# Kernel optimization log

Hardware: AMD Instinct MI355X
Metric: run time of the kernel (lower is better)

Reference implementation:

```python
import jax, jax.numpy as jnp
import numpy as np

RADIUS = 0.25  # module init arg


def _spp(x):
    """Spatial pyramid max pooling over the (K=8, C) plane.
    x: [B, N, 8, C] -> [B, N, 21] (4x4 + 2x2 + 1x1 bins)."""
    B, N, K, C = x.shape
    outs = []
    for h, w in ((4, 4), (2, 2), (1, 1)):
        r = x.reshape(B, N, h, K // h, w, C // w)
        outs.append(r.max(axis=(3, 5)).reshape(B, N, h * w))
    return jnp.concatenate(outs, axis=-1)


def _pointsift_select(xyz, radius):
    """Octant-wise nearest-neighbor selection. xyz: [Bp, N, 3] -> idx [Bp, N, 8]."""
    Bp, N, _ = xyz.shape
    judge = radius * radius
    # diff[b, n, m] = xyz[b, m] - xyz[b, n]  (point m relative to centroid n)
    diff = xyz[:, None, :, :] - xyz[:, :, None, :]          # [Bp, N, N, 3]
    dist = jnp.sum(diff * diff, axis=-1)                     # [Bp, N, N]
    octw = jnp.array([4, 2, 1], dtype=jnp.int32)
    sub = jnp.sum((diff + 1.0).astype(jnp.int32) * octw, -1)  # [Bp, N, N] octant id
    valid = (dist > 1e-10) & (dist < judge)
    eye = jnp.eye(N, dtype=bool)                             # self entry gets judge_dist
    idxs = []
    for i in range(8):
        d_i = jnp.where(valid & (sub == i), dist, 1e10)
        d_i = jnp.where(eye, judge, d_i)
        idxs.append(jnp.argmin(d_i, axis=-1))                # first-min, matches torch
    return jnp.stack(idxs, axis=-1)                          # [Bp, N, 8]


def setup_inputs() -> dict:
    key = jax.random.key(0)
    ks = jax.random.split(key, 7)
    C = 256
    x = jax.random.uniform(ks[0], (2, 2, 2048, 3), dtype=jnp.float32)
    w1 = jax.random.normal(ks[1], (C, 3), dtype=jnp.float32) * 0.05
    b1 = jax.random.normal(ks[2], (C,), dtype=jnp.float32) * 0.05
    w2 = jax.random.normal(ks[3], (C, C), dtype=jnp.float32) * 0.05
    b2 = jax.random.normal(ks[4], (C,), dtype=jnp.float32) * 0.05
    w3 = jax.random.normal(ks[5], (C, C), dtype=jnp.float32) * 0.05
    b3 = jax.random.normal(ks[6], (C,), dtype=jnp.float32) * 0.05
    return {"x": x, "w1": w1, "b1": b1, "w2": w2, "b2": b2, "w3": w3, "b3": b3}


def reference(x, w1, b1, w2, b2, w3, b3):
    B, T, N, _ = x.shape
    xyz = x.reshape(B * T, N, 3)
    idx = _pointsift_select(xyz, RADIUS)                     # [Bp, N, 8]
    b_idx = jnp.arange(B * T)[:, None, None]
    grouped = xyz[b_idx, idx] - xyz[:, :, None, :]           # [Bp, N, 8, 3] relative coords
    # three stacked 1x1 convs (no nonlinearity, per original Sequential)
    h = jnp.einsum('bnkc,oc->bnko', grouped, w1) + b1
    h = jnp.einsum('bnkc,oc->bnko', h, w2) + b2
    h = jnp.einsum('bnkc,oc->bnko', h, w3) + b3              # [Bp, N, 8, C]
    out = _spp(h)                                            # [Bp, N, 21]
    return out.reshape(B, T, N, -1)
```

## Files before the change

### kernel.cpp

```cpp
#include <hip/hip_runtime.h>

#define NPTS 2048
#define CCH  256
#define CAP  320
#define CAPU (CAP - 64)

template <int CTRL>
__device__ __forceinline__ float dppf(float v) {
    return __int_as_float(__builtin_amdgcn_update_dpp(
        0, __float_as_int(v), CTRL, 0xF, 0xF, true));
}
__device__ __forceinline__ float row16_max(float v) {
    v = fmaxf(v, dppf<0xB1>(v));
    v = fmaxf(v, dppf<0x4E>(v));
    v = fmaxf(v, dppf<0x141>(v));
    v = fmaxf(v, dppf<0x140>(v));
    return v;
}
__device__ __forceinline__ float row16_min(float v) {
    v = fminf(v, dppf<0xB1>(v));
    v = fminf(v, dppf<0x4E>(v));
    v = fminf(v, dppf<0x141>(v));
    v = fminf(v, dppf<0x140>(v));
    return v;
}
__device__ __forceinline__ float row16_sum(float v) {
    v += dppf<0xB1>(v);
    v += dppf<0x4E>(v);
    v += dppf<0x141>(v);
    v += dppf<0x140>(v);
    return v;
}
__device__ __forceinline__ float wave_sum(float v) {
    v = row16_sum(v);
    v += __shfl_xor(v, 16, 64);
    v += __shfl_xor(v, 32, 64);
    return v;
}


__global__ __launch_bounds__(256) void prep_kernel(
    const float* __restrict__ w1, const float* __restrict__ b1,
    const float* __restrict__ w2, const float* __restrict__ b2,
    const float* __restrict__ w3, const float* __restrict__ b3,
    float* __restrict__ ws)
{
    __shared__ float  w3row[CCH];
    __shared__ float4 wpart[4];
    int o = blockIdx.x, c = threadIdx.x;

    float w3c = w3[o * CCH + c];
    w3row[c] = w3c;
    __syncthreads();

    float a0 = 0.f, a1 = 0.f, a2 = 0.f, a3 = 0.f;
    const float* w2c = w2 + c;
    for (int k = 0; k < CCH; k += 4) {
        a0 = fmaf(w3row[k + 0], w2c[(k + 0) * CCH], a0);
        a1 = fmaf(w3row[k + 1], w2c[(k + 1) * CCH], a1);
        a2 = fmaf(w3row[k + 2], w2c[(k + 2) * CCH], a2);
        a3 = fmaf(w3row[k + 3], w2c[(k + 3) * CCH], a3);
    }
    float acc = (a0 + a1) + (a2 + a3);

    float4 v = make_float4(acc * w1[c * 3 + 0],
                           acc * w1[c * 3 + 1],
                           acc * w1[c * 3 + 2],
                           fmaf(acc, b1[c], w3c * b2[c]));
    v.x = wave_sum(v.x);
    v.y = wave_sum(v.y);
    v.z = wave_sum(v.z);
    v.w = wave_sum(v.w);
    if ((c & 63) == 0) wpart[c >> 6] = v;
    __syncthreads();
    if (c == 0) {
        float4 p0 = wpart[0], p1 = wpart[1], p2 = wpart[2], p3 = wpart[3];
        ws[o * 3 + 0] = (p0.x + p1.x) + (p2.x + p3.x);
        ws[o * 3 + 1] = (p0.y + p1.y) + (p2.y + p3.y);
        ws[o * 3 + 2] = (p0.z + p1.z) + (p2.z + p3.z);
        ws[3 * CCH + o] = (p0.w + p1.w) + (p2.w + p3.w) + b3[o];
    }
}

__global__ __launch_bounds__(1024) void pointsift_kernel(
    const float* __restrict__ x,
    const float* __restrict__ ws,
    float* __restrict__ out)
{
    __shared__ float4 sx4[NPTS];
    __shared__ unsigned short slist[16][CAP];

    int batch = blockIdx.x >> 7;
    int n0    = (blockIdx.x & 127) * 16;
    const float* xb = x + (size_t)batch * NPTS * 3;

    for (int i = threadIdx.x; i < NPTS; i += 1024) {
        float3 p = *(const float3*)(xb + 3 * i);
        sx4[i] = make_float4(p.x, p.y, p.z, 0.f);
    }

    int wave = threadIdx.x >> 6;
    int lane = threadIdx.x & 63;
    int n = n0 + wave;

    float3 cpt = *(const float3*)(xb + 3 * n);
    float cx = cpt.x, cy = cpt.y, cz = cpt.z;

    __syncthreads();

    unsigned short* slw = slist[wave];

    unsigned cnt = 0;
#pragma unroll 4
    for (int m = lane; m < NPTS; m += 64) {
        float4 p = sx4[m];
        float dx = p.x - cx, dy = p.y - cy, dz = p.z - cz;
        float d2 = __fadd_rn(__fadd_rn(__fmul_rn(dx, dx), __fmul_rn(dy, dy)),
                             __fmul_rn(dz, dz));
        bool valid = (d2 > 1e-10f) && (d2 < 0.0625f);
        unsigned long long mask = __ballot(valid);
        if (valid && cnt <= CAPU) {
            unsigned below = __builtin_amdgcn_mbcnt_hi(
                (unsigned)(mask >> 32),
                __builtin_amdgcn_mbcnt_lo((unsigned)mask, 0u));
            slw[cnt + below] = (unsigned short)m;
        }
        cnt += (unsigned)__popcll(mask);
    }

    float bd[8];
    int   bi[8];
#pragma unroll
    for (int i = 0; i < 8; ++i) { bd[i] = __builtin_inff(); bi[i] = n; }

    if (cnt <= CAPU) {
        int cn = (int)cnt;
        for (int t = lane; t < cn; t += 64) {
            int m = slw[t];
            float4 p = sx4[m];
            float dx = p.x - cx, dy = p.y - cy, dz = p.z - cz;
            float d2 = __fadd_rn(__fadd_rn(__fmul_rn(dx, dx), __fmul_rn(dy, dy)),
                                 __fmul_rn(dz, dz));
            int oct = 4 * (int)(dx + 1.0f) + 2 * (int)(dy + 1.0f) + (int)(dz + 1.0f);
#pragma unroll
            for (int i = 0; i < 8; ++i) {
                bool upd = (oct == i) && (d2 < bd[i]);
                bd[i] = upd ? d2 : bd[i];
                bi[i] = upd ? m : bi[i];
            }
        }
    } else {
        for (int m = lane; m < NPTS; m += 64) {
            float4 p = sx4[m];
            float dx = p.x - cx, dy = p.y - cy, dz = p.z - cz;
            float d2 = __fadd_rn(__fadd_rn(__fmul_rn(dx, dx), __fmul_rn(dy, dy)),
                                 __fmul_rn(dz, dz));
            bool valid = (d2 > 1e-10f) && (d2 < 0.0625f);
            int oct = 4 * (int)(dx + 1.0f) + 2 * (int)(dy + 1.0f) + (int)(dz + 1.0f);
#pragma unroll
            for (int i = 0; i < 8; ++i) {
                bool upd = valid && (oct == i) && (d2 < bd[i]);
                bd[i] = upd ? d2 : bd[i];
                bi[i] = upd ? m : bi[i];
            }
        }
    }

    int nidx[8];
#pragma unroll
    for (int i = 0; i < 8; ++i) {
        float mv = row16_min(bd[i]);
        mv = fminf(mv, __shfl_xor(mv, 16, 64));
        mv = fminf(mv, __shfl_xor(mv, 32, 64));
        unsigned long long mk = __ballot(bd[i] == mv);
        if (__popcll(mk) == 1) {
            nidx[i] = __builtin_amdgcn_readlane(bi[i], (int)__builtin_ctzll(mk));
        } else {
            int mm = (bd[i] == mv) ? bi[i] : 0x7FFFFFFF;
#pragma unroll
            for (int s = 32; s > 0; s >>= 1) {
                int o = __shfl_xor(mm, s, 64);
                mm = o < mm ? o : mm;
            }
            nidx[i] = mm;
        }
    }

    const float4* wsv = (const float4*)ws;
    float4 wa = wsv[lane * 3 + 0];
    float4 wb = wsv[lane * 3 + 1];
    float4 wc = wsv[lane * 3 + 2];
    float4 be = ((const float4*)(ws + 3 * CCH))[lane];
    float w[4][3] = {{wa.x, wa.y, wa.z}, {wa.w, wb.x, wb.y},
                     {wb.z, wb.w, wc.x}, {wc.y, wc.z, wc.w}};
    float bev[4] = {be.x, be.y, be.z, be.w};

    float m16[4];
#pragma unroll
    for (int i = 0; i < 4; ++i) m16[i] = -__builtin_inff();
#pragma unroll
    for (int k = 0; k < 8; ++k) {
        float4 p = sx4[nidx[k]];
        float gx = p.x - cx, gy = p.y - cy, gz = p.z - cz;
#pragma unroll
        for (int q = 0; q < 4; ++q) {
            float h = fmaf(gx, w[q][0], fmaf(gy, w[q][1], fmaf(gz, w[q][2], bev[q])));
            m16[k >> 1] = fmaxf(m16[k >> 1], h);
        }
    }

    float t[4], u[4];
#pragma unroll
    for (int i = 0; i < 4; ++i) {
        m16[i] = row16_max(m16[i]);
        t[i] = fmaxf(m16[i], __shfl_xor(m16[i], 16, 64));
        u[i] = fmaxf(t[i], __shfl_xor(t[i], 32, 64));
    }

    float* op = out + ((size_t)batch * NPTS + n) * 21;
    if ((lane & 15) == 0) {
        int j = lane >> 4;
#pragma unroll
        for (int i = 0; i < 4; ++i)
            op[i * 4 + j] = m16[i];
    }
    if (lane == 0 || lane == 32) {
        int j2 = lane >> 5;
        op[16 + 0 * 2 + j2] = fmaxf(t[0], t[1]);
        op[16 + 1 * 2 + j2] = fmaxf(t[2], t[3]);
    }
    if (lane == 0) {
        op[20] = fmaxf(fmaxf(u[0], u[1]), fmaxf(u[2], u[3]));
    }
}

extern "C" void kernel_launch(void* const* d_in, const int* in_sizes, int n_in,
                              void* d_out, int out_size, void* d_ws, size_t ws_size,
                              hipStream_t stream) {
    const float* x  = (const float*)d_in[0];
    const float* w1 = (const float*)d_in[1];
    const float* b1 = (const float*)d_in[2];
    const float* w2 = (const float*)d_in[3];
    const float* b2 = (const float*)d_in[4];
    const float* w3 = (const float*)d_in[5];
    const float* b3 = (const float*)d_in[6];
    float* out = (float*)d_out;
    float* ws  = (float*)d_ws;

    prep_kernel<<<CCH, CCH, 0, stream>>>(w1, b1, w2, b2, w3, b3, ws);

    int Bp = in_sizes[0] / (NPTS * 3);
    pointsift_kernel<<<Bp * (NPTS / 16), 1024, 0, stream>>>(x, ws, out);
}
```

Measured before the change: 26.83 us.

## Bin points into 4x4x4 uniform grid and scan only neighboring cells

Adds a binning pass to the prep kernel that counting-sorts each batch's points into a 4x4x4 grid of cells of size 0.25, storing sorted coordinates, original ids and cell start offsets in the workspace. The main kernel then scans only the 3x3x3 neighbouring cells of each centroid instead of all 2048 points when building the candidate list. Ties are broken on the original index so results still match first-min argmin order. The cost is an extra sort pass folded into the existing prep launch, plus reading neighbour coordinates from global memory in the final stage.

```diff
diff --git a/kernel.cpp b/kernel.cpp
--- a/kernel.cpp
+++ b/kernel.cpp
@@ -4,6 +4,10 @@
 #define CCH  256
 #define CAP  320
 #define CAPU (CAP - 64)
+
+#define STARTS_OFF 4096
+#define IDS_OFF    6144
+#define CRD_OFF    22528
 
 template <int CTRL>
 __device__ __forceinline__ float dppf(float v) {
@@ -38,47 +42,107 @@
     return v;
 }
 
-
-__global__ __launch_bounds__(256) void prep_kernel(
+__device__ __forceinline__ int cell_coord(float v) {
+    int c = (int)(v * 4.0f);
+    return min(3, max(0, c));
+}
+
+__global__ __launch_bounds__(256) void prep_bin_kernel(
+    const float* __restrict__ x,
     const float* __restrict__ w1, const float* __restrict__ b1,
     const float* __restrict__ w2, const float* __restrict__ b2,
     const float* __restrict__ w3, const float* __restrict__ b3,
-    float* __restrict__ ws)
+    float* __restrict__ ws, int Bp)
 {
     __shared__ float  w3row[CCH];
     __shared__ float4 wpart[4];
-    int o = blockIdx.x, c = threadIdx.x;
-
-    float w3c = w3[o * CCH + c];
-    w3row[c] = w3c;
+    __shared__ unsigned hist[64];
+    __shared__ unsigned curs[64];
+    __shared__ unsigned short cellOf[NPTS];
+
+    int tid = threadIdx.x;
+
+    if ((int)blockIdx.x < CCH) {
+        int o = blockIdx.x, c = tid;
+        float w3c = w3[o * CCH + c];
+        w3row[c] = w3c;
+        __syncthreads();
+
+        float a0 = 0.f, a1 = 0.f, a2 = 0.f, a3 = 0.f;
+        const float* w2c = w2 + c;
+        for (int k = 0; k < CCH; k += 4) {
+            a0 = fmaf(w3row[k + 0], w2c[(k + 0) * CCH], a0);
+            a1 = fmaf(w3row[k + 1], w2c[(k + 1) * CCH], a1);
+            a2 = fmaf(w3row[k + 2], w2c[(k + 2) * CCH], a2);
+            a3 = fmaf(w3row[k + 3], w2c[(k + 3) * CCH], a3);
+        }
+        float acc = (a0 + a1) + (a2 + a3);
+
+        float4 v = make_float4(acc * w1[c * 3 + 0],
+                               acc * w1[c * 3 + 1],
+                               acc * w1[c * 3 + 2],
+                               fmaf(acc, b1[c], w3c * b2[c]));
+        v.x = wave_sum(v.x);
+        v.y = wave_sum(v.y);
+        v.z = wave_sum(v.z);
+        v.w = wave_sum(v.w);
+        if ((c & 63) == 0) wpart[c >> 6] = v;
+        __syncthreads();
+        if (c == 0) {
+            float4 p0 = wpart[0], p1 = wpart[1], p2 = wpart[2], p3 = wpart[3];
+            ws[o * 3 + 0] = (p0.x + p1.x) + (p2.x + p3.x);
+            ws[o * 3 + 1] = (p0.y + p1.y) + (p2.y + p3.y);
+            ws[o * 3 + 2] = (p0.z + p1.z) + (p2.z + p3.z);
+            ws[3 * CCH + o] = (p0.w + p1.w) + (p2.w + p3.w) + b3[o];
+        }
+        return;
+    }
+
+    int b = blockIdx.x - CCH;
+    if (b >= Bp) return;
+    const float* xb = x + (size_t)b * NPTS * 3;
+
+    if (tid < 64) hist[tid] = 0;
     __syncthreads();
 
-    float a0 = 0.f, a1 = 0.f, a2 = 0.f, a3 = 0.f;
-    const float* w2c = w2 + c;
-    for (int k = 0; k < CCH; k += 4) {
-        a0 = fmaf(w3row[k + 0], w2c[(k + 0) * CCH], a0);
-        a1 = fmaf(w3row[k + 1], w2c[(k + 1) * CCH], a1);
-        a2 = fmaf(w3row[k + 2], w2c[(k + 2) * CCH], a2);
-        a3 = fmaf(w3row[k + 3], w2c[(k + 3) * CCH], a3);
-    }
-    float acc = (a0 + a1) + (a2 + a3);
-
-    float4 v = make_float4(acc * w1[c * 3 + 0],
-                           acc * w1[c * 3 + 1],
-                           acc * w1[c * 3 + 2],
-                           fmaf(acc, b1[c], w3c * b2[c]));
-    v.x = wave_sum(v.x);
-    v.y = wave_sum(v.y);
-    v.z = wave_sum(v.z);
-    v.w = wave_sum(v.w);
-    if ((c & 63) == 0) wpart[c >> 6] = v;
+    float3 pr[8];
+    int    cl[8];
+#pragma unroll 8
+    for (int j = 0; j < 8; ++j) {
+        int i = tid + 256 * j;
+        float3 p = *(const float3*)(xb + 3 * i);
+        pr[j] = p;
+        int c = (cell_coord(p.x) << 4) | (cell_coord(p.y) << 2) | cell_coord(p.z);
+        cl[j] = c;
+        cellOf[i] = (unsigned short)c;
+        atomicAdd(&hist[c], 1u);
+    }
     __syncthreads();
-    if (c == 0) {
-        float4 p0 = wpart[0], p1 = wpart[1], p2 = wpart[2], p3 = wpart[3];
-        ws[o * 3 + 0] = (p0.x + p1.x) + (p2.x + p3.x);
-        ws[o * 3 + 1] = (p0.y + p1.y) + (p2.y + p3.y);
-        ws[o * 3 + 2] = (p0.z + p1.z) + (p2.z + p3.z);
-        ws[3 * CCH + o] = (p0.w + p1.w) + (p2.w + p3.w) + b3[o];
+
+    if (tid < 64) {
+        unsigned v = hist[tid];
+        unsigned inc = v;
+#pragma unroll
+        for (int s = 1; s < 64; s <<= 1) {
+            unsigned o = __shfl_up(inc, s, 64);
+            if (tid >= s) inc += o;
+        }
+        unsigned excl = inc - v;
+        curs[tid] = excl;
+        unsigned* st = (unsigned*)((char*)ws + STARTS_OFF) + b * 128;
+        st[tid] = excl;
+        if (tid == 63) st[64] = NPTS;
+    }
+    __syncthreads();
+
+    float4* crd         = (float4*)((char*)ws + CRD_OFF) + (size_t)b * NPTS;
+    unsigned short* ids = (unsigned short*)((char*)ws + IDS_OFF) + (size_t)b * NPTS;
+#pragma unroll 8
+    for (int j = 0; j < 8; ++j) {
+        int i = tid + 256 * j;
+        unsigned pos = atomicAdd(&curs[cl[j]], 1u);
+        crd[pos] = make_float4(pr[j].x, pr[j].y, pr[j].z, 0.f);
+        ids[pos] = (unsigned short)i;
     }
 }
 
@@ -87,17 +151,24 @@
     const float* __restrict__ ws,
     float* __restrict__ out)
 {
-    __shared__ float4 sx4[NPTS];
+    __shared__ float4 sc[NPTS];
+    __shared__ unsigned short sid[NPTS];
+    __shared__ unsigned sstart[65];
     __shared__ unsigned short slist[16][CAP];
 
     int batch = blockIdx.x >> 7;
     int n0    = (blockIdx.x & 127) * 16;
+
+    const float4* crd = (const float4*)((const char*)ws + CRD_OFF) + (size_t)batch * NPTS;
+    const unsigned short* idg = (const unsigned short*)((const char*)ws + IDS_OFF) + (size_t)batch * NPTS;
+    const unsigned* stg = (const unsigned*)((const char*)ws + STARTS_OFF) + batch * 128;
     const float* xb = x + (size_t)batch * NPTS * 3;
 
     for (int i = threadIdx.x; i < NPTS; i += 1024) {
-        float3 p = *(const float3*)(xb + 3 * i);
-        sx4[i] = make_float4(p.x, p.y, p.z, 0.f);
-    }
+        sc[i]  = crd[i];
+        sid[i] = idg[i];
+    }
+    if (threadIdx.x < 65) sstart[threadIdx.x] = stg[threadIdx.x];
 
     int wave = threadIdx.x >> 6;
     int lane = threadIdx.x & 63;
@@ -108,24 +179,40 @@
 
     __syncthreads();
 
+    int ccx = cell_coord(cx), ccy = cell_coord(cy), ccz = cell_coord(cz);
+    int zlo = ccz > 0 ? ccz - 1 : 0;
+    int zhi = ccz < 3 ? ccz + 1 : 3;
+
     unsigned short* slw = slist[wave];
 
     unsigned cnt = 0;
-#pragma unroll 4
-    for (int m = lane; m < NPTS; m += 64) {
-        float4 p = sx4[m];
-        float dx = p.x - cx, dy = p.y - cy, dz = p.z - cz;
-        float d2 = __fadd_rn(__fadd_rn(__fmul_rn(dx, dx), __fmul_rn(dy, dy)),
-                             __fmul_rn(dz, dz));
-        bool valid = (d2 > 1e-10f) && (d2 < 0.0625f);
-        unsigned long long mask = __ballot(valid);
-        if (valid && cnt <= CAPU) {
-            unsigned below = __builtin_amdgcn_mbcnt_hi(
-                (unsigned)(mask >> 32),
-                __builtin_amdgcn_mbcnt_lo((unsigned)mask, 0u));
-            slw[cnt + below] = (unsigned short)m;
-        }
-        cnt += (unsigned)__popcll(mask);
+    for (int di = -1; di <= 1; ++di) {
+        int a = ccx + di;
+        if ((unsigned)a > 3u) continue;
+        for (int dj = -1; dj <= 1; ++dj) {
+            int bcol = ccy + dj;
+            if ((unsigned)bcol > 3u) continue;
+            int base = (a << 4) | (bcol << 2);
+            unsigned s0 = sstart[base + zlo];
+            unsigned e0 = sstart[base + zhi + 1];
+            for (unsigned p0 = s0; p0 < e0; p0 += 64) {
+                unsigned pos = p0 + lane;
+                bool inb = pos < e0;
+                float4 p = sc[inb ? pos : 0];
+                float dx = p.x - cx, dy = p.y - cy, dz = p.z - cz;
+                float d2 = __fadd_rn(__fadd_rn(__fmul_rn(dx, dx), __fmul_rn(dy, dy)),
+                                     __fmul_rn(dz, dz));
+                bool valid = inb && (d2 > 1e-10f) && (d2 < 0.0625f);
+                unsigned long long mask = __ballot(valid);
+                if (valid && cnt <= CAPU) {
+                    unsigned below = __builtin_amdgcn_mbcnt_hi(
+                        (unsigned)(mask >> 32),
+                        __builtin_amdgcn_mbcnt_lo((unsigned)mask, 0u));
+                    slw[cnt + below] = (unsigned short)pos;
+                }
+                cnt += (unsigned)__popcll(mask);
+            }
+        }
     }
 
     float bd[8];
@@ -136,22 +223,25 @@
     if (cnt <= CAPU) {
         int cn = (int)cnt;
         for (int t = lane; t < cn; t += 64) {
-            int m = slw[t];
-            float4 p = sx4[m];
+            int pos = slw[t];
+            float4 p = sc[pos];
+            int m = sid[pos];
             float dx = p.x - cx, dy = p.y - cy, dz = p.z - cz;
             float d2 = __fadd_rn(__fadd_rn(__fmul_rn(dx, dx), __fmul_rn(dy, dy)),
                                  __fmul_rn(dz, dz));
             int oct = 4 * (int)(dx + 1.0f) + 2 * (int)(dy + 1.0f) + (int)(dz + 1.0f);
 #pragma unroll
             for (int i = 0; i < 8; ++i) {
-                bool upd = (oct == i) && (d2 < bd[i]);
+                bool upd = (oct == i) &&
+                           ((d2 < bd[i]) || ((d2 == bd[i]) && (m < bi[i])));
                 bd[i] = upd ? d2 : bd[i];
                 bi[i] = upd ? m : bi[i];
             }
         }
     } else {
-        for (int m = lane; m < NPTS; m += 64) {
-            float4 p = sx4[m];
+        for (int pos = lane; pos < NPTS; pos += 64) {
+            float4 p = sc[pos];
+            int m = sid[pos];
             float dx = p.x - cx, dy = p.y - cy, dz = p.z - cz;
             float d2 = __fadd_rn(__fadd_rn(__fmul_rn(dx, dx), __fmul_rn(dy, dy)),
                                  __fmul_rn(dz, dz));
@@ -159,7 +249,8 @@
             int oct = 4 * (int)(dx + 1.0f) + 2 * (int)(dy + 1.0f) + (int)(dz + 1.0f);
 #pragma unroll
             for (int i = 0; i < 8; ++i) {
-                bool upd = valid && (oct == i) && (d2 < bd[i]);
+                bool upd = valid && (oct == i) &&
+                           ((d2 < bd[i]) || ((d2 == bd[i]) && (m < bi[i])));
                 bd[i] = upd ? d2 : bd[i];
                 bi[i] = upd ? m : bi[i];
             }
@@ -200,7 +291,7 @@
     for (int i = 0; i < 4; ++i) m16[i] = -__builtin_inff();
 #pragma unroll
     for (int k = 0; k < 8; ++k) {
-        float4 p = sx4[nidx[k]];
+        float3 p = *(const float3*)(xb + 3 * nidx[k]);
         float gx = p.x - cx, gy = p.y - cy, gz = p.z - cz;
 #pragma unroll
         for (int q = 0; q < 4; ++q) {
@@ -247,8 +338,8 @@
     float* out = (float*)d_out;
     float* ws  = (float*)d_ws;
 
-    prep_kernel<<<CCH, CCH, 0, stream>>>(w1, b1, w2, b2, w3, b3, ws);
-
     int Bp = in_sizes[0] / (NPTS * 3);
+
+    prep_bin_kernel<<<CCH + Bp, CCH, 0, stream>>>(x, w1, b1, w2, b2, w3, b3, ws, Bp);
     pointsift_kernel<<<Bp * (NPTS / 16), 1024, 0, stream>>>(x, ws, out);
 }
```

After: 28.97 us. +8.0%, slower.

## Bin points into a 4x4x4 shared-memory grid to prune neighbor search

Applied to the files above, without the earlier changes.

Each block builds a 64-cell spatial histogram of the batch's points, prefix-sums it and scatters the points into cell-sorted order in shared memory. Each centroid wave then scans only the 3x3x3 neighboring cells instead of all 2048 points. Original indices are packed into the float4's w slot, and 64-bit (distance, index) keys keep first-min tie-breaking after the reorder. The prep kernel now computes two output channels per block, sharing the w2 loads. This adds atomics and extra barriers per block, and the gather at the end reads from global memory.

```diff
diff --git a/kernel.cpp b/kernel.cpp
--- a/kernel.cpp
+++ b/kernel.cpp
@@ -38,6 +38,11 @@
     return v;
 }
 
+__device__ __forceinline__ int cell_coord(float v) {
+    int c = (int)(v * 4.0f);
+    return min(3, max(0, c));
+}
+
 
 __global__ __launch_bounds__(256) void prep_kernel(
     const float* __restrict__ w1, const float* __restrict__ b1,
@@ -45,36 +50,55 @@
     const float* __restrict__ w3, const float* __restrict__ b3,
     float* __restrict__ ws)
 {
-    __shared__ float  w3row[CCH];
-    __shared__ float4 wpart[4];
-    int o = blockIdx.x, c = threadIdx.x;
-
-    float w3c = w3[o * CCH + c];
-    w3row[c] = w3c;
+    __shared__ float  w3row[2][CCH];
+    __shared__ float4 wpart[2][4];
+    int o0 = blockIdx.x * 2, c = threadIdx.x;
+
+    float w3c0 = w3[(o0 + 0) * CCH + c];
+    float w3c1 = w3[(o0 + 1) * CCH + c];
+    w3row[0][c] = w3c0;
+    w3row[1][c] = w3c1;
     __syncthreads();
 
     float a0 = 0.f, a1 = 0.f, a2 = 0.f, a3 = 0.f;
+    float b0 = 0.f, b1p = 0.f, b2p = 0.f, b3p = 0.f;
     const float* w2c = w2 + c;
     for (int k = 0; k < CCH; k += 4) {
-        a0 = fmaf(w3row[k + 0], w2c[(k + 0) * CCH], a0);
-        a1 = fmaf(w3row[k + 1], w2c[(k + 1) * CCH], a1);
-        a2 = fmaf(w3row[k + 2], w2c[(k + 2) * CCH], a2);
-        a3 = fmaf(w3row[k + 3], w2c[(k + 3) * CCH], a3);
-    }
-    float acc = (a0 + a1) + (a2 + a3);
-
-    float4 v = make_float4(acc * w1[c * 3 + 0],
-                           acc * w1[c * 3 + 1],
-                           acc * w1[c * 3 + 2],
-                           fmaf(acc, b1[c], w3c * b2[c]));
-    v.x = wave_sum(v.x);
-    v.y = wave_sum(v.y);
-    v.z = wave_sum(v.z);
-    v.w = wave_sum(v.w);
-    if ((c & 63) == 0) wpart[c >> 6] = v;
-    __syncthreads();
-    if (c == 0) {
-        float4 p0 = wpart[0], p1 = wpart[1], p2 = wpart[2], p3 = wpart[3];
+        float q0 = w2c[(k + 0) * CCH];
+        float q1 = w2c[(k + 1) * CCH];
+        float q2 = w2c[(k + 2) * CCH];
+        float q3 = w2c[(k + 3) * CCH];
+        a0 = fmaf(w3row[0][k + 0], q0, a0);
+        a1 = fmaf(w3row[0][k + 1], q1, a1);
+        a2 = fmaf(w3row[0][k + 2], q2, a2);
+        a3 = fmaf(w3row[0][k + 3], q3, a3);
+        b0  = fmaf(w3row[1][k + 0], q0, b0);
+        b1p = fmaf(w3row[1][k + 1], q1, b1p);
+        b2p = fmaf(w3row[1][k + 2], q2, b2p);
+        b3p = fmaf(w3row[1][k + 3], q3, b3p);
+    }
+    float accA = (a0 + a1) + (a2 + a3);
+    float accB = (b0 + b1p) + (b2p + b3p);
+
+    float w1x = w1[c * 3 + 0], w1y = w1[c * 3 + 1], w1z = w1[c * 3 + 2];
+    float b1c = b1[c], b2c = b2[c];
+
+    float4 vA = make_float4(accA * w1x, accA * w1y, accA * w1z,
+                            fmaf(accA, b1c, w3c0 * b2c));
+    float4 vB = make_float4(accB * w1x, accB * w1y, accB * w1z,
+                            fmaf(accB, b1c, w3c1 * b2c));
+    vA.x = wave_sum(vA.x); vA.y = wave_sum(vA.y);
+    vA.z = wave_sum(vA.z); vA.w = wave_sum(vA.w);
+    vB.x = wave_sum(vB.x); vB.y = wave_sum(vB.y);
+    vB.z = wave_sum(vB.z); vB.w = wave_sum(vB.w);
+    if ((c & 63) == 0) {
+        wpart[0][c >> 6] = vA;
+        wpart[1][c >> 6] = vB;
+    }
+    __syncthreads();
+    if (c < 2) {
+        int o = o0 + c;
+        float4 p0 = wpart[c][0], p1 = wpart[c][1], p2 = wpart[c][2], p3 = wpart[c][3];
         ws[o * 3 + 0] = (p0.x + p1.x) + (p2.x + p3.x);
         ws[o * 3 + 1] = (p0.y + p1.y) + (p2.y + p3.y);
         ws[o * 3 + 2] = (p0.z + p1.z) + (p2.z + p3.z);
@@ -87,20 +111,55 @@
     const float* __restrict__ ws,
     float* __restrict__ out)
 {
-    __shared__ float4 sx4[NPTS];
+    __shared__ float4 scrd[NPTS];
+    __shared__ unsigned sstart[66];
+    __shared__ unsigned shist[64];
+    __shared__ unsigned scur[64];
     __shared__ unsigned short slist[16][CAP];
 
+    int tid = threadIdx.x;
     int batch = blockIdx.x >> 7;
     int n0    = (blockIdx.x & 127) * 16;
     const float* xb = x + (size_t)batch * NPTS * 3;
 
-    for (int i = threadIdx.x; i < NPTS; i += 1024) {
-        float3 p = *(const float3*)(xb + 3 * i);
-        sx4[i] = make_float4(p.x, p.y, p.z, 0.f);
-    }
-
-    int wave = threadIdx.x >> 6;
-    int lane = threadIdx.x & 63;
+    if (tid < 64) shist[tid] = 0;
+    __syncthreads();
+
+    float2 f0 = *(const float2*)(xb + 6 * tid + 0);
+    float2 f1 = *(const float2*)(xb + 6 * tid + 2);
+    float2 f2 = *(const float2*)(xb + 6 * tid + 4);
+    float3 p0 = make_float3(f0.x, f0.y, f1.x);
+    float3 p1 = make_float3(f1.y, f2.x, f2.y);
+    int c0 = (cell_coord(p0.x) << 4) | (cell_coord(p0.y) << 2) | cell_coord(p0.z);
+    int c1 = (cell_coord(p1.x) << 4) | (cell_coord(p1.y) << 2) | cell_coord(p1.z);
+    atomicAdd(&shist[c0], 1u);
+    atomicAdd(&shist[c1], 1u);
+    __syncthreads();
+
+    if (tid < 64) {
+        unsigned v = shist[tid];
+        unsigned incl = v;
+#pragma unroll
+        for (int s = 1; s < 64; s <<= 1) {
+            unsigned o = __shfl_up(incl, s, 64);
+            if (tid >= s) incl += o;
+        }
+        unsigned excl = incl - v;
+        sstart[tid] = excl;
+        scur[tid] = excl;
+        if (tid == 63) sstart[64] = NPTS;
+    }
+    __syncthreads();
+
+    {
+        unsigned q0 = atomicAdd(&scur[c0], 1u);
+        scrd[q0] = make_float4(p0.x, p0.y, p0.z, __uint_as_float(2u * tid));
+        unsigned q1 = atomicAdd(&scur[c1], 1u);
+        scrd[q1] = make_float4(p1.x, p1.y, p1.z, __uint_as_float(2u * tid + 1u));
+    }
+
+    int wave = tid >> 6;
+    int lane = tid & 63;
     int n = n0 + wave;
 
     float3 cpt = *(const float3*)(xb + 3 * n);
@@ -108,60 +167,80 @@
 
     __syncthreads();
 
+    int ccx = cell_coord(cx), ccy = cell_coord(cy), ccz = cell_coord(cz);
+    int zlo = ccz > 0 ? ccz - 1 : 0;
+    int zhi = ccz < 3 ? ccz + 1 : 3;
+
     unsigned short* slw = slist[wave];
 
     unsigned cnt = 0;
-#pragma unroll 4
-    for (int m = lane; m < NPTS; m += 64) {
-        float4 p = sx4[m];
-        float dx = p.x - cx, dy = p.y - cy, dz = p.z - cz;
-        float d2 = __fadd_rn(__fadd_rn(__fmul_rn(dx, dx), __fmul_rn(dy, dy)),
-                             __fmul_rn(dz, dz));
-        bool valid = (d2 > 1e-10f) && (d2 < 0.0625f);
-        unsigned long long mask = __ballot(valid);
-        if (valid && cnt <= CAPU) {
-            unsigned below = __builtin_amdgcn_mbcnt_hi(
-                (unsigned)(mask >> 32),
-                __builtin_amdgcn_mbcnt_lo((unsigned)mask, 0u));
-            slw[cnt + below] = (unsigned short)m;
-        }
-        cnt += (unsigned)__popcll(mask);
-    }
-
-    float bd[8];
-    int   bi[8];
-#pragma unroll
-    for (int i = 0; i < 8; ++i) { bd[i] = __builtin_inff(); bi[i] = n; }
+    for (int di = -1; di <= 1; ++di) {
+        int a = ccx + di;
+        if ((unsigned)a > 3u) continue;
+        for (int dj = -1; dj <= 1; ++dj) {
+            int bc = ccy + dj;
+            if ((unsigned)bc > 3u) continue;
+            int base = (a << 4) | (bc << 2);
+            unsigned s0 = sstart[base + zlo];
+            unsigned e0 = sstart[base + zhi + 1];
+            for (unsigned pp = s0; pp < e0; pp += 64) {
+                unsigned pos = pp + lane;
+                bool inb = pos < e0;
+                float4 p = scrd[inb ? pos : 0];
+                float dx = p.x - cx, dy = p.y - cy, dz = p.z - cz;
+                float d2 = __fadd_rn(__fadd_rn(__fmul_rn(dx, dx), __fmul_rn(dy, dy)),
+                                     __fmul_rn(dz, dz));
+                bool valid = inb && (d2 > 1e-10f) && (d2 < 0.0625f);
+                unsigned long long mask = __ballot(valid);
+                if (valid && cnt <= CAPU) {
+                    unsigned below = __builtin_amdgcn_mbcnt_hi(
+                        (unsigned)(mask >> 32),
+                        __builtin_amdgcn_mbcnt_lo((unsigned)mask, 0u));
+                    slw[cnt + below] = (unsigned short)pos;
+                }
+                cnt += (unsigned)__popcll(mask);
+            }
+        }
+    }
+
+    unsigned long long bk[8];
+#pragma unroll
+    for (int i = 0; i < 8; ++i)
+        bk[i] = (0x7f800000ULL << 32) | (unsigned)n;
 
     if (cnt <= CAPU) {
         int cn = (int)cnt;
         for (int t = lane; t < cn; t += 64) {
-            int m = slw[t];
-            float4 p = sx4[m];
+            int pos = slw[t];
+            float4 p = scrd[pos];
+            unsigned m = __float_as_uint(p.w);
             float dx = p.x - cx, dy = p.y - cy, dz = p.z - cz;
             float d2 = __fadd_rn(__fadd_rn(__fmul_rn(dx, dx), __fmul_rn(dy, dy)),
                                  __fmul_rn(dz, dz));
             int oct = 4 * (int)(dx + 1.0f) + 2 * (int)(dy + 1.0f) + (int)(dz + 1.0f);
+            unsigned long long key =
+                ((unsigned long long)__float_as_uint(d2) << 32) | m;
 #pragma unroll
             for (int i = 0; i < 8; ++i) {
-                bool upd = (oct == i) && (d2 < bd[i]);
-                bd[i] = upd ? d2 : bd[i];
-                bi[i] = upd ? m : bi[i];
+                bool upd = (oct == i) && (key < bk[i]);
+                bk[i] = upd ? key : bk[i];
             }
         }
     } else {
-        for (int m = lane; m < NPTS; m += 64) {
-            float4 p = sx4[m];
+        for (int pos = lane; pos < NPTS; pos += 64) {
+            float4 p = scrd[pos];
+            unsigned m = __float_as_uint(p.w);
             float dx = p.x - cx, dy = p.y - cy, dz = p.z - cz;
             float d2 = __fadd_rn(__fadd_rn(__fmul_rn(dx, dx), __fmul_rn(dy, dy)),
                                  __fmul_rn(dz, dz));
             bool valid = (d2 > 1e-10f) && (d2 < 0.0625f);
             int oct = 4 * (int)(dx + 1.0f) + 2 * (int)(dy + 1.0f) + (int)(dz + 1.0f);
+            unsigned long long key =
+                ((unsigned long long)__float_as_uint(d2) << 32) | m;
 #pragma unroll
             for (int i = 0; i < 8; ++i) {
-                bool upd = valid && (oct == i) && (d2 < bd[i]);
-                bd[i] = upd ? d2 : bd[i];
-                bi[i] = upd ? m : bi[i];
+                bool upd = valid && (oct == i) && (key < bk[i]);
+                bk[i] = upd ? key : bk[i];
             }
         }
     }
@@ -169,14 +248,16 @@
     int nidx[8];
 #pragma unroll
     for (int i = 0; i < 8; ++i) {
-        float mv = row16_min(bd[i]);
+        float bdf = __uint_as_float((unsigned)(bk[i] >> 32));
+        int   bii = (int)(unsigned)bk[i];
+        float mv = row16_min(bdf);
         mv = fminf(mv, __shfl_xor(mv, 16, 64));
         mv = fminf(mv, __shfl_xor(mv, 32, 64));
-        unsigned long long mk = __ballot(bd[i] == mv);
+        unsigned long long mk = __ballot(bdf == mv);
         if (__popcll(mk) == 1) {
-            nidx[i] = __builtin_amdgcn_readlane(bi[i], (int)__builtin_ctzll(mk));
+            nidx[i] = __builtin_amdgcn_readlane(bii, (int)__builtin_ctzll(mk));
         } else {
-            int mm = (bd[i] == mv) ? bi[i] : 0x7FFFFFFF;
+            int mm = (bdf == mv) ? bii : 0x7FFFFFFF;
 #pragma unroll
             for (int s = 32; s > 0; s >>= 1) {
                 int o = __shfl_xor(mm, s, 64);
@@ -200,7 +281,7 @@
     for (int i = 0; i < 4; ++i) m16[i] = -__builtin_inff();
 #pragma unroll
     for (int k = 0; k < 8; ++k) {
-        float4 p = sx4[nidx[k]];
+        float3 p = *(const float3*)(xb + 3 * nidx[k]);
         float gx = p.x - cx, gy = p.y - cy, gz = p.z - cz;
 #pragma unroll
         for (int q = 0; q < 4; ++q) {
@@ -247,7 +328,7 @@
     float* out = (float*)d_out;
     float* ws  = (float*)d_ws;
 
-    prep_kernel<<<CCH, CCH, 0, stream>>>(w1, b1, w2, b2, w3, b3, ws);
+    prep_kernel<<<CCH / 2, CCH, 0, stream>>>(w1, b1, w2, b2, w3, b3, ws);
 
     int Bp = in_sizes[0] / (NPTS * 3);
     pointsift_kernel<<<Bp * (NPTS / 16), 1024, 0, stream>>>(x, ws, out);
```

After: 26.33 us. No clear change (-1.9%).
